# Optimization experiments

Hardware: AMD Instinct MI355X
Metric: run time of the kernel (lower is better)

## Reference

```python
import jax, jax.numpy as jnp
import numpy as np

D = 1024      # decoder_embed_dim
H = 16        # retention heads
DK = D // H   # q/k head dim = 64
DV = 2 * D // H  # value head dim = 128 (value_embed_dim = 2*embed_dim)
L = 3         # decoder layers
FFN = 4096
S = 1024      # seq len = Lx*Ly
B = 4
V = 2         # vocab
EPS = 1e-6


def layer_norm(x, s, b):
    m = x.mean(-1, keepdims=True)
    v = ((x - m) ** 2).mean(-1, keepdims=True)
    return (x - m) / jnp.sqrt(v + 1e-5) * s + b


def rotate_every_two(x):
    x1 = x[..., ::2]
    x2 = x[..., 1::2]
    return jnp.stack([-x2, x1], axis=-1).reshape(x.shape)


def rel_pos():
    # xpos-style rotary angles + per-head decay mask (torchscale RetNetRelPos)
    angle = 1.0 / (10000.0 ** jnp.linspace(0.0, 1.0, DK // 2))
    angle = jnp.stack([angle, angle], axis=-1).reshape(-1)  # [DK]
    idx = jnp.arange(S)
    sin = jnp.sin(idx[:, None] * angle[None, :])  # [S, DK]
    cos = jnp.cos(idx[:, None] * angle[None, :])
    gamma = 1.0 - 2.0 ** (-5.0 - jnp.arange(H, dtype=jnp.float32))  # [H]
    n = idx[:, None]
    m = idx[None, :]
    expo = jnp.where(n >= m, (n - m).astype(jnp.float32), 0.0)
    dmask = jnp.where(n >= m, gamma[:, None, None] ** expo[None], 0.0)  # [H,S,S]
    dmask = dmask / jnp.sqrt(dmask.sum(-1, keepdims=True))  # row-normalize
    dmask = jnp.nan_to_num(dmask)
    return sin, cos, dmask


def msr(x, Wq, Wk, Wv, Wg, Wo, sin, cos, dmask):
    # multi-scale retention, parallel form
    b, s, _ = x.shape
    q = (x @ Wq).reshape(b, s, H, DK)
    k = (x @ Wk).reshape(b, s, H, DK) * (DK ** -0.5)
    v = (x @ Wv).reshape(b, s, H, DV)
    c = cos[None, :, None, :]
    sn = sin[None, :, None, :]
    q = q * c + rotate_every_two(q) * sn
    k = k * c + rotate_every_two(k) * sn
    qk = jnp.einsum('bnhd,bmhd->bhnm', q, k) * dmask[None]  # [B,H,S,S]
    qk = qk / jnp.clip(jnp.abs(qk).sum(-1, keepdims=True), 1.0, None)
    o = jnp.einsum('bhnm,bmhd->bnhd', qk, v)  # [B,S,H,DV]
    # per-head RMS group norm, no affine
    o = o / jnp.sqrt((o ** 2).mean(-1, keepdims=True) + EPS)
    o = o.reshape(b, s, H * DV)
    o = jax.nn.silu(x @ Wg) * o  # swish gate
    return o @ Wo


def reference(tokens, emb, Wq, Wk, Wv, Wg, Wo, ln1_s, ln1_b, ln2_s, ln2_b,
              W1, b1, W2, b2, lnf_s, lnf_b, Wout):
    shifted = jnp.concatenate(
        [jnp.zeros((tokens.shape[0], 1), tokens.dtype), tokens[:, :-1]], axis=1)
    h = emb[shifted] * jnp.sqrt(jnp.float32(D))
    sin, cos, dmask = rel_pos()
    for l in range(L):
        h = h + msr(layer_norm(h, ln1_s[l], ln1_b[l]),
                    Wq[l], Wk[l], Wv[l], Wg[l], Wo[l], sin, cos, dmask)
        z = layer_norm(h, ln2_s[l], ln2_b[l])
        h = h + (jax.nn.gelu(z @ W1[l] + b1[l]) @ W2[l] + b2[l])
    h = layer_norm(h, lnf_s, lnf_b)
    logits = h @ Wout  # [B,S,V]
    return jax.nn.log_softmax(logits, axis=-1)


def setup_inputs() -> dict:
    key = jax.random.key(0)
    ks = jax.random.split(key, 12)
    sd = 0.02
    return {
        'tokens': jax.random.randint(ks[0], (B, S), 0, V),
        'emb': jax.random.normal(ks[1], (V, D), jnp.float32) * sd,
        'Wq': jax.random.normal(ks[2], (L, D, D), jnp.float32) * sd,
        'Wk': jax.random.normal(ks[3], (L, D, D), jnp.float32) * sd,
        'Wv': jax.random.normal(ks[4], (L, D, 2 * D), jnp.float32) * sd,
        'Wg': jax.random.normal(ks[5], (L, D, 2 * D), jnp.float32) * sd,
        'Wo': jax.random.normal(ks[6], (L, 2 * D, D), jnp.float32) * sd,
        'ln1_s': jnp.ones((L, D), jnp.float32),
        'ln1_b': jnp.zeros((L, D), jnp.float32),
        'ln2_s': jnp.ones((L, D), jnp.float32),
        'ln2_b': jnp.zeros((L, D), jnp.float32),
        'W1': jax.random.normal(ks[7], (L, D, FFN), jnp.float32) * sd,
        'b1': jnp.zeros((L, FFN), jnp.float32),
        'W2': jax.random.normal(ks[8], (L, FFN, D), jnp.float32) * sd,
        'b2': jnp.zeros((L, D), jnp.float32),
        'lnf_s': jnp.ones((D,), jnp.float32),
        'lnf_b': jnp.zeros((D,), jnp.float32),
        'Wout': jax.random.normal(ks[9], (D, V), jnp.float32) * sd,
    }
```

## Files before the change

### kernel.cpp

```cpp
#include <hip/hip_runtime.h>
#include <hip/hip_bf16.h>
#include <math.h>
#include <stdint.h>

#define D_   1024
#define H_   16
#define DK_  64
#define DV_  128
#define L_   3
#define FFN_ 4096
#define S_   1024
#define B_   4
#define NF_  6144

typedef __attribute__((ext_vector_type(8))) _Float16 f16x8;
typedef __attribute__((ext_vector_type(4))) _Float16 f16x4;
typedef __attribute__((ext_vector_type(4))) float f32x4;

__device__ __forceinline__ void gl2lds16(const void* g, void* l) {
    __builtin_amdgcn_global_load_lds(
        (const __attribute__((address_space(1))) void*)(uintptr_t)g,
        (__attribute__((address_space(3))) void*)(uintptr_t)l, 16, 0, 0);
}
#define MFMA16(a,b,c) __builtin_amdgcn_mfma_f32_16x16x32_f16(a,b,c,0,0,0)

__device__ __forceinline__ float fast_gelu(float v) {
    float y = 1.5957691216f * (v + 0.044715f * v * v * v);
    return v * (1.0f / (1.0f + __expf(-y)));
}

__device__ __forceinline__ void tile_swizzle(int pid, int N, int* m0, int* n0) {
    int nb = N >> 7;
    int sgn = nb >> 3;
    int sid = pid >> 6, wi = pid & 63;
    int smi = sid / sgn, sni = sid - smi * sgn;
    *m0 = ((smi << 3) + (wi >> 3)) << 7;
    *n0 = ((sni << 3) + (wi & 7)) << 7;
}

__global__ __launch_bounds__(256) void k_embed(const int* __restrict__ tokens,
                                               const float* __restrict__ emb,
                                               float* __restrict__ h) {
    int i = blockIdx.x * 256 + threadIdx.x;
    int d  = i & (D_ - 1);
    int bs = i >> 10;
    int s  = bs & (S_ - 1);
    int b  = bs >> 10;
    int tok = (s == 0) ? 0 : tokens[b * S_ + s - 1];
    h[i] = emb[tok * D_ + d] * 32.0f;
}

__global__ __launch_bounds__(256) void k_ln(float* __restrict__ x,
                                            const float* __restrict__ p0,
                                            const float* __restrict__ p1,
                                            int np,
                                            const float* __restrict__ s,
                                            const float* __restrict__ b,
                                            _Float16* __restrict__ y) {
    int row = blockIdx.x;
    int t = threadIdx.x;
    size_t base = (size_t)row * D_ + t * 4;
    float4 xv = *(float4*)&x[base];
    if (np) {
        float4 a = *(const float4*)&p0[base];
        float4 c = *(const float4*)&p1[base];
        xv.x += a.x + c.x; xv.y += a.y + c.y;
        xv.z += a.z + c.z; xv.w += a.w + c.w;
        *(float4*)&x[base] = xv;
    }
    float sum = xv.x + xv.y + xv.z + xv.w;
    float ssq = xv.x * xv.x + xv.y * xv.y + xv.z * xv.z + xv.w * xv.w;
    __shared__ float sm1[4], sm2[4];
    #pragma unroll
    for (int off = 32; off > 0; off >>= 1) {
        sum += __shfl_down(sum, off, 64);
        ssq += __shfl_down(ssq, off, 64);
    }
    int lane = t & 63, w = t >> 6;
    if (lane == 0) { sm1[w] = sum; sm2[w] = ssq; }
    __syncthreads();
    sum = sm1[0] + sm1[1] + sm1[2] + sm1[3];
    ssq = sm2[0] + sm2[1] + sm2[2] + sm2[3];
    float mean = sum * (1.0f / D_);
    float var  = ssq * (1.0f / D_) - mean * mean;
    float inv  = 1.0f / sqrtf(var + 1e-5f);
    float4 sv = *(const float4*)&s[t * 4];
    float4 bv = *(const float4*)&b[t * 4];
    f16x4 o;
    o.x = (_Float16)((xv.x - mean) * inv * sv.x + bv.x);
    o.y = (_Float16)((xv.y - mean) * inv * sv.y + bv.y);
    o.z = (_Float16)((xv.z - mean) * inv * sv.z + bv.z);
    o.w = (_Float16)((xv.w - mean) * inv * sv.w + bv.w);
    *(f16x4*)&y[base] = o;
}

__global__ __launch_bounds__(256) void k_wcast(const float* __restrict__ in,
                                               _Float16* __restrict__ out,
                                               int K, int N) {
    __shared__ float Ts[32][33];
    int n0 = blockIdx.x * 32, k0 = blockIdx.y * 32;
    int t = threadIdx.x;
    #pragma unroll
    for (int c = 0; c < 4; c++) {
        int e = c * 256 + t; int kr = e >> 5, nc = e & 31;
        Ts[kr][nc] = in[(size_t)(k0 + kr) * N + n0 + nc];
    }
    __syncthreads();
    #pragma unroll
    for (int c = 0; c < 4; c++) {
        int e = c * 256 + t; int nr = e >> 5, kc = e & 31;
        out[(size_t)(n0 + nr) * K + k0 + kc] = (_Float16)Ts[kc][nr];
    }
}

__global__ __launch_bounds__(256) void k_gemm_mfma(
    const _Float16* __restrict__ A, const _Float16* __restrict__ Bt,
    const float* __restrict__ bias, float* __restrict__ Cf,
    _Float16* __restrict__ Ch, int M, int N, int K, int flags)
{
    __shared__ __attribute__((aligned(16))) _Float16 As[128 * 32];
    __shared__ __attribute__((aligned(16))) _Float16 Bs[128 * 32];
    int t = threadIdx.x;
    int m0, n0;
    tile_swizzle(blockIdx.x, N, &m0, &n0);
    int w = t >> 6, lane = t & 63;
    int quad = lane >> 4, l16 = lane & 15;
    int wm = (w >> 1) * 64, wn = (w & 1) * 64;
    const f16x8* aptr[4]; const f16x8* bptr[4];
    #pragma unroll
    for (int i = 0; i < 4; i++) {
        int ra = wm + i * 16 + l16;
        aptr[i] = (const f16x8*)&As[ra * 32 + ((quad ^ ((ra >> 1) & 3)) * 8)];
        int rb = wn + i * 16 + l16;
        bptr[i] = (const f16x8*)&Bs[rb * 32 + ((quad ^ ((rb >> 1) & 3)) * 8)];
    }
    f32x4 acc[4][4] = {};
    for (int k0 = 0; k0 < K; k0 += 32) {
        __syncthreads();
        #pragma unroll
        for (int c = 0; c < 2; c++) {
            int chunk = c * 256 + t;
            int row = chunk >> 2, cg = chunk & 3;
            int ko = (cg ^ ((row >> 1) & 3)) * 8;
            gl2lds16(A  + (size_t)(m0 + row) * K + k0 + ko, As + chunk * 8);
            gl2lds16(Bt + (size_t)(n0 + row) * K + k0 + ko, Bs + chunk * 8);
        }
        __syncthreads();
        f16x8 af[4], bfr[4];
        #pragma unroll
        for (int i = 0; i < 4; i++) af[i] = *aptr[i];
        #pragma unroll
        for (int j = 0; j < 4; j++) bfr[j] = *bptr[j];
        #pragma unroll
        for (int i = 0; i < 4; i++)
            #pragma unroll
            for (int j = 0; j < 4; j++)
                acc[i][j] = MFMA16(af[i], bfr[j], acc[i][j]);
    }
    #pragma unroll
    for (int i = 0; i < 4; i++) {
        #pragma unroll
        for (int r = 0; r < 4; r++) {
            int row = m0 + wm + i * 16 + quad * 4 + r;
            #pragma unroll
            for (int j = 0; j < 4; j++) {
                int col = n0 + wn + j * 16 + l16;
                float v = acc[i][j][r];
                if (flags & 2) v += bias[col];
                if (flags & 4) v = fast_gelu(v);
                if (flags & 8) Ch[(size_t)row * N + col] = (_Float16)v;
                else Cf[(size_t)row * N + col] = v;
            }
        }
    }
}

__global__ __launch_bounds__(256) void k_gemm_splitk(
    const _Float16* __restrict__ A, const _Float16* __restrict__ Bt,
    const float* __restrict__ bias, float* __restrict__ P,
    int M, int N, int K, int Kc)
{
    __shared__ __attribute__((aligned(16))) _Float16 As[128 * 32];
    __shared__ __attribute__((aligned(16))) _Float16 Bs[128 * 32];
    int t = threadIdx.x;
    int m0, n0;
    tile_swizzle(blockIdx.x, N, &m0, &n0);
    int kc = blockIdx.z;
    const _Float16* Ac  = A  + (size_t)kc * Kc;
    const _Float16* Btc = Bt + (size_t)kc * Kc;
    float* Pz = P + (size_t)kc * M * N;
    int w = t >> 6, lane = t & 63;
    int quad = lane >> 4, l16 = lane & 15;
    int wm = (w >> 1) * 64, wn = (w & 1) * 64;
    const f16x8* aptr[4]; const f16x8* bptr[4];
    #pragma unroll
    for (int i = 0; i < 4; i++) {
        int ra = wm + i * 16 + l16;
        aptr[i] = (const f16x8*)&As[ra * 32 + ((quad ^ ((ra >> 1) & 3)) * 8)];
        int rb = wn + i * 16 + l16;
        bptr[i] = (const f16x8*)&Bs[rb * 32 + ((quad ^ ((rb >> 1) & 3)) * 8)];
    }
    f32x4 acc[4][4] = {};
    for (int k0 = 0; k0 < Kc; k0 += 32) {
        __syncthreads();
        #pragma unroll
        for (int c = 0; c < 2; c++) {
            int chunk = c * 256 + t;
            int row = chunk >> 2, cg = chunk & 3;
            int ko = (cg ^ ((row >> 1) & 3)) * 8;
            gl2lds16(Ac  + (size_t)(m0 + row) * K + k0 + ko, As + chunk * 8);
            gl2lds16(Btc + (size_t)(n0 + row) * K + k0 + ko, Bs + chunk * 8);
        }
        __syncthreads();
        f16x8 af[4], bfr[4];
        #pragma unroll
        for (int i = 0; i < 4; i++) af[i] = *aptr[i];
        #pragma unroll
        for (int j = 0; j < 4; j++) bfr[j] = *bptr[j];
        #pragma unroll
        for (int i = 0; i < 4; i++)
            #pragma unroll
            for (int j = 0; j < 4; j++)
                acc[i][j] = MFMA16(af[i], bfr[j], acc[i][j]);
    }
    bool addb = (kc == 0) && (bias != nullptr);
    #pragma unroll
    for (int i = 0; i < 4; i++) {
        #pragma unroll
        for (int r = 0; r < 4; r++) {
            int row = m0 + wm + i * 16 + quad * 4 + r;
            #pragma unroll
            for (int j = 0; j < 4; j++) {
                int col = n0 + wn + j * 16 + l16;
                float v = acc[i][j][r];
                if (addb) v += bias[col];
                Pz[(size_t)row * N + col] = v;
            }
        }
    }
}

__global__ __launch_bounds__(256) void k_rope(_Float16* __restrict__ x, float scale) {
    int i = blockIdx.x * 256 + threadIdx.x;
    int pair = i & 31;
    int hh = (i >> 5) & 15;
    int bs = i >> 9;
    int sIdx = bs & (S_ - 1);
    float ang = expf(-(float)pair * (1.0f / 31.0f) * 9.210340372f);
    float ph = (float)sIdx * ang;
    float sn, cs;
    sincosf(ph, &sn, &cs);
    size_t base = (size_t)bs * NF_ + hh * DK_ + 2 * pair;
    float x1 = (float)x[base], x2 = (float)x[base + 1];
    x[base]     = (_Float16)((x1 * cs - x2 * sn) * scale);
    x[base + 1] = (_Float16)((x2 * cs + x1 * sn) * scale);
}

__global__ __launch_bounds__(256) void k_vtrans(const _Float16* __restrict__ vb,
                                                _Float16* __restrict__ Vt) {
    int st = blockIdx.x, dt = blockIdx.y, bh = blockIdx.z;
    int hh = bh & 15, b = bh >> 4;
    __shared__ __attribute__((aligned(16))) _Float16 Ts[64][72];
    int t = threadIdx.x;
    const _Float16* src = vb + (size_t)(b * S_ + st * 64) * NF_ + 2048 + hh * DV_ + dt * 64;
    #pragma unroll
    for (int c = 0; c < 2; c++) {
        int chunk = c * 256 + t;
        int r = chunk >> 3, co = (chunk & 7) * 8;
        *(f16x8*)&Ts[r][co] = *(const f16x8*)(src + (size_t)r * NF_ + co);
    }
    __syncthreads();
    _Float16* dst = Vt + ((size_t)bh * DV_ + dt * 64) * S_ + st * 64;
    #pragma unroll
    for (int c = 0; c < 2; c++) {
        int chunk = c * 256 + t;
        int dr = chunk >> 3, so = (chunk & 7) * 8;
        f16x8 val;
        #pragma unroll
        for (int j = 0; j < 8; j++) val[j] = Ts[so + j][dr];
        *(f16x8*)(dst + (size_t)dr * S_ + so) = val;
    }
}

__global__ __launch_bounds__(256) void k_attn(const _Float16* __restrict__ qkvg,
                                              const _Float16* __restrict__ Vt,
                                              float* __restrict__ of) {
    int nt = blockIdx.x, bh = blockIdx.y;
    int hh = bh & 15, b = bh >> 4;
    int t = threadIdx.x, w = t >> 6, lane = t & 63;
    int quad = lane >> 4, l16 = lane & 15;
    int n0 = nt * 64;

    __shared__ __attribute__((aligned(16))) _Float16 Qs[64 * 64];
    __shared__ __attribute__((aligned(16))) _Float16 Ks[64 * 64];
    __shared__ __attribute__((aligned(16))) _Float16 Vs[128 * 64];
    __shared__ __attribute__((aligned(16))) _Float16 Ss[64 * 64];

    const _Float16* qg = qkvg + (size_t)(b * S_ + n0) * NF_ + hh * DK_;
    const _Float16* kg = qkvg + (size_t)(b * S_) * NF_ + 1024 + hh * DK_;
    const _Float16* vg = Vt + (size_t)bh * DV_ * S_;

    #pragma unroll
    for (int c = 0; c < 2; c++) {
        int chunk = c * 256 + t;
        int r = chunk >> 3, cg = chunk & 7;
        int ko = (cg ^ (r & 7)) * 8;
        gl2lds16(qg + (size_t)r * NF_ + ko, Qs + chunk * 8);
    }
    double gd   = 1.0 - exp2((double)(-5 - hh));
    double l2gd = log2(gd);
    float  l2g  = (float)l2gd;
    float rn[4];
    #pragma unroll
    for (int r = 0; r < 4; r++) {
        int n = n0 + w * 16 + quad * 4 + r;
        double rowsum = (1.0 - exp2(l2gd * (double)(n + 1))) / (1.0 - gd);
        rn[r] = (float)(1.0 / sqrt(rowsum));
    }
    int ra = w * 16 + l16;
    const f16x8* qp0 = (const f16x8*)&Qs[ra * 64 + (( quad      ^ (ra & 7)) * 8)];
    const f16x8* qp1 = (const f16x8*)&Qs[ra * 64 + (((quad + 4) ^ (ra & 7)) * 8)];
    const f16x8* sp0 = (const f16x8*)&Ss[ra * 64 + (( quad      ^ (ra & 7)) * 8)];
    const f16x8* sp1 = (const f16x8*)&Ss[ra * 64 + (((quad + 4) ^ (ra & 7)) * 8)];
    const f16x8* kp0[4]; const f16x8* kp1[4];
    const f16x8* vp0[8]; const f16x8* vp1[8];
    #pragma unroll
    for (int j = 0; j < 4; j++) {
        int rb = j * 16 + l16;
        kp0[j] = (const f16x8*)&Ks[rb * 64 + (( quad      ^ (rb & 7)) * 8)];
        kp1[j] = (const f16x8*)&Ks[rb * 64 + (((quad + 4) ^ (rb & 7)) * 8)];
    }
    #pragma unroll
    for (int j = 0; j < 8; j++) {
        int rv = j * 16 + l16;
        vp0[j] = (const f16x8*)&Vs[rv * 64 + (( quad      ^ (rv & 7)) * 8)];
        vp1[j] = (const f16x8*)&Vs[rv * 64 + (((quad + 4) ^ (rv & 7)) * 8)];
    }
    f32x4 oacc[8] = {};
    float absAcc[4] = {};

    for (int mt = 0; mt <= nt; mt++) {
        int m0 = mt * 64;
        __syncthreads();
        #pragma unroll
        for (int c = 0; c < 2; c++) {
            int chunk = c * 256 + t;
            int r = chunk >> 3, cg = chunk & 7;
            int ko = (cg ^ (r & 7)) * 8;
            gl2lds16(kg + (size_t)(m0 + r) * NF_ + ko, Ks + chunk * 8);
        }
        #pragma unroll
        for (int c = 0; c < 4; c++) {
            int chunk = c * 256 + t;
            int r = chunk >> 3, cg = chunk & 7;
            int ko = (cg ^ (r & 7)) * 8;
            gl2lds16(vg + (size_t)r * S_ + m0 + ko, Vs + chunk * 8);
        }
        __syncthreads();
        f16x8 a0 = *qp0, a1 = *qp1;
        f32x4 sacc[4] = {};
        #pragma unroll
        for (int j = 0; j < 4; j++) {
            sacc[j] = MFMA16(a0, *kp0[j], sacc[j]);
            sacc[j] = MFMA16(a1, *kp1[j], sacc[j]);
        }
        #pragma unroll
        for (int j = 0; j < 4; j++) {
            int m = m0 + j * 16 + l16;
            #pragma unroll
            for (int r = 0; r < 4; r++) {
                int n = n0 + w * 16 + quad * 4 + r;
                float dm = (n >= m) ? exp2f((float)(n - m) * l2g) * rn[r] : 0.0f;
                float sv = sacc[j][r] * dm;
                absAcc[r] += fabsf(sv);
                int rowS = w * 16 + quad * 4 + r;
                int colS = j * 16 + l16;
                Ss[rowS * 64 + ((((colS >> 3) ^ (rowS & 7)) << 3) | (colS & 7))] = (_Float16)sv;
            }
        }
        __syncthreads();
        f16x8 s0 = *sp0, s1 = *sp1;
        #pragma unroll
        for (int j = 0; j < 8; j++) {
            oacc[j] = MFMA16(s0, *vp0[j], oacc[j]);
            oacc[j] = MFMA16(s1, *vp1[j], oacc[j]);
        }
    }
    #pragma unroll
    for (int r = 0; r < 4; r++) {
        float s_ = absAcc[r];
        #pragma unroll
        for (int off = 1; off < 16; off <<= 1) s_ += __shfl_xor(s_, off, 64);
        absAcc[r] = s_;
    }
    #pragma unroll
    for (int r = 0; r < 4; r++) {
        int n = n0 + w * 16 + quad * 4 + r;
        float sc = 1.0f / fmaxf(absAcc[r], 1.0f);
        float* og = of + (size_t)(b * S_ + n) * (H_ * DV_) + hh * DV_;
        #pragma unroll
        for (int j = 0; j < 8; j++)
            og[j * 16 + l16] = oacc[j][r] * sc;
    }
}

__global__ __launch_bounds__(256) void k_rmsgate(const float* __restrict__ o,
                                                 const _Float16* __restrict__ qkvg,
                                                 _Float16* __restrict__ out) {
    int row = blockIdx.x * 2 + (threadIdx.x >> 7);
    int tc = threadIdx.x & 127;
    int bs = row >> 4, hh = row & 15;
    size_t obase = (size_t)row * 128 + tc;
    float val = o[obase];
    float gv  = (float)qkvg[(size_t)bs * NF_ + 4096 + hh * DV_ + tc];
    float ss = val * val;
    #pragma unroll
    for (int off = 32; off > 0; off >>= 1) ss += __shfl_down(ss, off, 64);
    __shared__ float sm[4];
    int wv = threadIdx.x >> 6;
    if ((threadIdx.x & 63) == 0) sm[wv] = ss;
    __syncthreads();
    int rw = (threadIdx.x >> 7) * 2;
    ss = sm[rw] + sm[rw + 1];
    float rms = 1.0f / sqrtf(ss * (1.0f / 128.0f) + 1e-6f);
    float sig = 1.0f / (1.0f + __expf(-gv));
    out[obase] = (_Float16)(gv * sig * val * rms);
}

__global__ __launch_bounds__(256) void k_final(const float* __restrict__ x,
                                               const float* __restrict__ p0,
                                               const float* __restrict__ p1,
                                               const float* __restrict__ s,
                                               const float* __restrict__ b,
                                               const float* __restrict__ Wout,
                                               float* __restrict__ out) {
    int row = blockIdx.x;
    int t = threadIdx.x;
    size_t base = (size_t)row * D_ + t * 4;
    float4 xv = *(const float4*)&x[base];
    {
        float4 a = *(const float4*)&p0[base];
        float4 c = *(const float4*)&p1[base];
        xv.x += a.x + c.x; xv.y += a.y + c.y;
        xv.z += a.z + c.z; xv.w += a.w + c.w;
    }
    float sum = xv.x + xv.y + xv.z + xv.w;
    float ssq = xv.x * xv.x + xv.y * xv.y + xv.z * xv.z + xv.w * xv.w;
    __shared__ float sm1[4], sm2[4];
    #pragma unroll
    for (int off = 32; off > 0; off >>= 1) {
        sum += __shfl_down(sum, off, 64);
        ssq += __shfl_down(ssq, off, 64);
    }
    int lane = t & 63, w = t >> 6;
    if (lane == 0) { sm1[w] = sum; sm2[w] = ssq; }
    __syncthreads();
    sum = sm1[0] + sm1[1] + sm1[2] + sm1[3];
    ssq = sm2[0] + sm2[1] + sm2[2] + sm2[3];
    float mean = sum * (1.0f / D_);
    float var  = ssq * (1.0f / D_) - mean * mean;
    float inv  = 1.0f / sqrtf(var + 1e-5f);
    float4 sv = *(const float4*)&s[t * 4];
    float4 bv = *(const float4*)&b[t * 4];
    float ln[4];
    ln[0] = (xv.x - mean) * inv * sv.x + bv.x;
    ln[1] = (xv.y - mean) * inv * sv.y + bv.y;
    ln[2] = (xv.z - mean) * inv * sv.z + bv.z;
    ln[3] = (xv.w - mean) * inv * sv.w + bv.w;
    float l0 = 0.0f, l1 = 0.0f;
    #pragma unroll
    for (int i = 0; i < 4; i++) {
        int d = t * 4 + i;
        l0 += ln[i] * Wout[d * 2 + 0];
        l1 += ln[i] * Wout[d * 2 + 1];
    }
    #pragma unroll
    for (int off = 32; off > 0; off >>= 1) {
        l0 += __shfl_down(l0, off, 64);
        l1 += __shfl_down(l1, off, 64);
    }
    __syncthreads();
    if (lane == 0) { sm1[w] = l0; sm2[w] = l1; }
    __syncthreads();
    if (t == 0) {
        l0 = sm1[0] + sm1[1] + sm1[2] + sm1[3];
        l1 = sm2[0] + sm2[1] + sm2[2] + sm2[3];
        float mx  = fmaxf(l0, l1);
        float lse = mx + logf(expf(l0 - mx) + expf(l1 - mx));
        out[(size_t)row * 2 + 0] = l0 - lse;
        out[(size_t)row * 2 + 1] = l1 - lse;
    }
}

extern "C" void kernel_launch(void* const* d_in, const int* in_sizes, int n_in,
                              void* d_out, int out_size, void* d_ws, size_t ws_size,
                              hipStream_t stream) {
    const int*   tokens = (const int*)d_in[0];
    const float* emb    = (const float*)d_in[1];
    const float* Wq     = (const float*)d_in[2];
    const float* Wk     = (const float*)d_in[3];
    const float* Wv     = (const float*)d_in[4];
    const float* Wg     = (const float*)d_in[5];
    const float* Wo     = (const float*)d_in[6];
    const float* ln1_s  = (const float*)d_in[7];
    const float* ln1_b  = (const float*)d_in[8];
    const float* ln2_s  = (const float*)d_in[9];
    const float* ln2_b  = (const float*)d_in[10];
    const float* W1     = (const float*)d_in[11];
    const float* b1     = (const float*)d_in[12];
    const float* W2     = (const float*)d_in[13];
    const float* b2     = (const float*)d_in[14];
    const float* lnf_s  = (const float*)d_in[15];
    const float* lnf_b  = (const float*)d_in[16];
    const float* Wout   = (const float*)d_in[17];

    float* ws = (float*)d_ws;
    const size_t M1 = 1u << 20;
    float*     h    = ws;
    _Float16*  x1h  = (_Float16*)(ws + 4 * M1);
    _Float16*  whb  = (_Float16*)(ws + 6 * M1);
    _Float16*  wQKVG= whb;
    _Float16*  woT  = whb + 6 * M1;
    _Float16*  w1T  = whb + 8 * M1;
    _Float16*  w2T  = whb + 12 * M1;
    _Float16*  qkvg = (_Float16*)(ws + 14 * M1);
    _Float16*  Vth  = (_Float16*)(ws + 27 * M1);
    float*     of   = ws + 31 * M1;
    _Float16*  oh   = (_Float16*)(ws + 27 * M1);
    _Float16*  f1h  = (_Float16*)(ws + 14 * M1);
    float*     pb0  = ws + 31 * M1;
    float*     pb1  = ws + 35 * M1;

    k_embed<<<16384, 256, 0, stream>>>(tokens, emb, h);

    for (int l = 0; l < L_; l++) {
        const float* pWq = Wq + (size_t)l * M1;
        const float* pWk = Wk + (size_t)l * M1;
        const float* pWv = Wv + (size_t)l * 2 * M1;
        const float* pWg = Wg + (size_t)l * 2 * M1;
        const float* pWo = Wo + (size_t)l * 2 * M1;
        const float* pW1 = W1 + (size_t)l * 4 * M1;
        const float* pW2 = W2 + (size_t)l * 4 * M1;

        k_wcast<<<dim3(32, 32),  256, 0, stream>>>(pWq, wQKVG,          1024, 1024);
        k_wcast<<<dim3(32, 32),  256, 0, stream>>>(pWk, wQKVG + 1 * M1, 1024, 1024);
        k_wcast<<<dim3(64, 32),  256, 0, stream>>>(pWv, wQKVG + 2 * M1, 1024, 2048);
        k_wcast<<<dim3(64, 32),  256, 0, stream>>>(pWg, wQKVG + 4 * M1, 1024, 2048);
        k_wcast<<<dim3(32, 64),  256, 0, stream>>>(pWo, woT, 2048, 1024);
        k_wcast<<<dim3(128, 32), 256, 0, stream>>>(pW1, w1T, 1024, 4096);
        k_wcast<<<dim3(32, 128), 256, 0, stream>>>(pW2, w2T, 4096, 1024);

        k_ln<<<4096, 256, 0, stream>>>(h, pb0, pb1, (l == 0) ? 0 : 1,
                                       ln1_s + l * D_, ln1_b + l * D_, x1h);
        k_gemm_mfma<<<dim3(1536), 256, 0, stream>>>(x1h, wQKVG, nullptr, nullptr, qkvg,
                                                    4096, NF_, 1024, 8);
        k_rope<<<8192, 256, 0, stream>>>(qkvg, 1.0f);
        k_rope<<<8192, 256, 0, stream>>>(qkvg + 1024, 0.125f);
        k_vtrans<<<dim3(16, 2, 64), 256, 0, stream>>>(qkvg, Vth);
        k_attn<<<dim3(16, 64), 256, 0, stream>>>(qkvg, Vth, of);
        k_rmsgate<<<32768, 256, 0, stream>>>(of, qkvg, oh);
        k_gemm_splitk<<<dim3(256, 1, 2), 256, 0, stream>>>(oh, woT, nullptr, pb0,
                                                           4096, 1024, 2048, 1024);
        k_ln<<<4096, 256, 0, stream>>>(h, pb0, pb1, 1,
                                       ln2_s + l * D_, ln2_b + l * D_, x1h);
        k_gemm_mfma<<<dim3(1024), 256, 0, stream>>>(x1h, w1T, b1 + l * FFN_, nullptr, f1h,
                                                    4096, 4096, 1024, 2 | 4 | 8);
        k_gemm_splitk<<<dim3(256, 1, 2), 256, 0, stream>>>(f1h, w2T, b2 + l * D_, pb0,
                                                           4096, 1024, 4096, 2048);
    }
    k_final<<<4096, 256, 0, stream>>>(h, pb0, pb1, lnf_s, lnf_b, Wout, (float*)d_out);
}
```

Before: 1.459 ms.

## Fuse rope into QKV GEMM, rmsgate into attention, residual into output GEMMs

```diff
diff --git a/kernel.cpp b/kernel.cpp
--- a/kernel.cpp
+++ b/kernel.cpp
@@ -50,24 +50,14 @@
     h[i] = emb[tok * D_ + d] * 32.0f;
 }
 
-__global__ __launch_bounds__(256) void k_ln(float* __restrict__ x,
-                                            const float* __restrict__ p0,
-                                            const float* __restrict__ p1,
-                                            int np,
+__global__ __launch_bounds__(256) void k_ln(const float* __restrict__ x,
                                             const float* __restrict__ s,
                                             const float* __restrict__ b,
                                             _Float16* __restrict__ y) {
     int row = blockIdx.x;
     int t = threadIdx.x;
     size_t base = (size_t)row * D_ + t * 4;
-    float4 xv = *(float4*)&x[base];
-    if (np) {
-        float4 a = *(const float4*)&p0[base];
-        float4 c = *(const float4*)&p1[base];
-        xv.x += a.x + c.x; xv.y += a.y + c.y;
-        xv.z += a.z + c.z; xv.w += a.w + c.w;
-        *(float4*)&x[base] = xv;
-    }
+    float4 xv = *(const float4*)&x[base];
     float sum = xv.x + xv.y + xv.z + xv.w;
     float ssq = xv.x * xv.x + xv.y * xv.y + xv.z * xv.z + xv.w * xv.w;
     __shared__ float sm1[4], sm2[4];
@@ -94,6 +84,34 @@
     *(f16x4*)&y[base] = o;
 }
 
+__global__ __launch_bounds__(256) void k_wcast4(const float* __restrict__ wq,
+                                                const float* __restrict__ wk,
+                                                const float* __restrict__ wv,
+                                                const float* __restrict__ wg,
+                                                _Float16* __restrict__ dst) {
+    int bid = blockIdx.x;
+    const float* src; _Float16* out; int N; int local;
+    if (bid < 1024)      { src = wq; out = dst;                 N = 1024; local = bid; }
+    else if (bid < 2048) { src = wk; out = dst + 1024 * 1024;   N = 1024; local = bid - 1024; }
+    else if (bid < 4096) { src = wv; out = dst + 2*1024*1024;   N = 2048; local = bid - 2048; }
+    else                 { src = wg; out = dst + 4*1024*1024;   N = 2048; local = bid - 4096; }
+    int ntiles = N >> 5;
+    int n0 = (local % ntiles) * 32, k0 = (local / ntiles) * 32;
+    __shared__ float Ts[32][33];
+    int t = threadIdx.x;
+    #pragma unroll
+    for (int c = 0; c < 4; c++) {
+        int e = c * 256 + t; int kr = e >> 5, nc = e & 31;
+        Ts[kr][nc] = src[(size_t)(k0 + kr) * N + n0 + nc];
+    }
+    __syncthreads();
+    #pragma unroll
+    for (int c = 0; c < 4; c++) {
+        int e = c * 256 + t; int nr = e >> 5, kc = e & 31;
+        out[(size_t)(n0 + nr) * 1024 + k0 + kc] = (_Float16)Ts[kc][nr];
+    }
+}
+
 __global__ __launch_bounds__(256) void k_wcast(const float* __restrict__ in,
                                                _Float16* __restrict__ out,
                                                int K, int N) {
@@ -115,8 +133,8 @@
 
 __global__ __launch_bounds__(256) void k_gemm_mfma(
     const _Float16* __restrict__ A, const _Float16* __restrict__ Bt,
-    const float* __restrict__ bias, float* __restrict__ Cf,
-    _Float16* __restrict__ Ch, int M, int N, int K, int flags)
+    const float* __restrict__ bias, _Float16* __restrict__ Ch,
+    int M, int N, int K, int flags)
 {
     __shared__ __attribute__((aligned(16))) _Float16 As[128 * 32];
     __shared__ __attribute__((aligned(16))) _Float16 Bs[128 * 32];
@@ -168,64 +186,78 @@
                 float v = acc[i][j][r];
                 if (flags & 2) v += bias[col];
                 if (flags & 4) v = fast_gelu(v);
-                if (flags & 8) Ch[(size_t)row * N + col] = (_Float16)v;
-                else Cf[(size_t)row * N + col] = v;
+                if (flags & 16) {
+                    if (col < 2048) {
+                        int p = (col & 63) >> 1;
+                        int srow = row & (S_ - 1);
+                        float ang = __expf(-(float)p * (1.0f / 31.0f) * 9.210340372f);
+                        float ph = (float)srow * ang;
+                        float sn, cs;
+                        __sincosf(ph, &sn, &cs);
+                        float partner = __shfl_xor(v, 1, 64);
+                        v = (l16 & 1) ? (v * cs + partner * sn)
+                                      : (v * cs - partner * sn);
+                        if (col >= 1024) v *= 0.125f;
+                    }
+                }
+                Ch[(size_t)row * N + col] = (_Float16)v;
             }
         }
     }
 }
 
-__global__ __launch_bounds__(256) void k_gemm_splitk(
+__global__ __launch_bounds__(256) void k_gemm_rmw(
     const _Float16* __restrict__ A, const _Float16* __restrict__ Bt,
-    const float* __restrict__ bias, float* __restrict__ P,
-    int M, int N, int K, int Kc)
+    const float* __restrict__ bias, float* __restrict__ Cf,
+    int M, int N, int K)
 {
-    __shared__ __attribute__((aligned(16))) _Float16 As[128 * 32];
+    __shared__ __attribute__((aligned(16))) _Float16 As[64 * 32];
     __shared__ __attribute__((aligned(16))) _Float16 Bs[128 * 32];
     int t = threadIdx.x;
-    int m0, n0;
-    tile_swizzle(blockIdx.x, N, &m0, &n0);
-    int kc = blockIdx.z;
-    const _Float16* Ac  = A  + (size_t)kc * Kc;
-    const _Float16* Btc = Bt + (size_t)kc * Kc;
-    float* Pz = P + (size_t)kc * M * N;
+    int n0 = blockIdx.x * 128, m0 = blockIdx.y * 64;
     int w = t >> 6, lane = t & 63;
     int quad = lane >> 4, l16 = lane & 15;
-    int wm = (w >> 1) * 64, wn = (w & 1) * 64;
-    const f16x8* aptr[4]; const f16x8* bptr[4];
-    #pragma unroll
-    for (int i = 0; i < 4; i++) {
+    int wm = (w >> 1) * 32, wn = (w & 1) * 64;
+    const f16x8* aptr[2]; const f16x8* bptr[4];
+    #pragma unroll
+    for (int i = 0; i < 2; i++) {
         int ra = wm + i * 16 + l16;
         aptr[i] = (const f16x8*)&As[ra * 32 + ((quad ^ ((ra >> 1) & 3)) * 8)];
-        int rb = wn + i * 16 + l16;
-        bptr[i] = (const f16x8*)&Bs[rb * 32 + ((quad ^ ((rb >> 1) & 3)) * 8)];
-    }
-    f32x4 acc[4][4] = {};
-    for (int k0 = 0; k0 < Kc; k0 += 32) {
-        __syncthreads();
+    }
+    #pragma unroll
+    for (int j = 0; j < 4; j++) {
+        int rb = wn + j * 16 + l16;
+        bptr[j] = (const f16x8*)&Bs[rb * 32 + ((quad ^ ((rb >> 1) & 3)) * 8)];
+    }
+    f32x4 acc[2][4] = {};
+    for (int k0 = 0; k0 < K; k0 += 32) {
+        __syncthreads();
+        {
+            int row = t >> 2, cg = t & 3;
+            int ko = (cg ^ ((row >> 1) & 3)) * 8;
+            gl2lds16(A + (size_t)(m0 + row) * K + k0 + ko, As + t * 8);
+        }
         #pragma unroll
         for (int c = 0; c < 2; c++) {
             int chunk = c * 256 + t;
             int row = chunk >> 2, cg = chunk & 3;
             int ko = (cg ^ ((row >> 1) & 3)) * 8;
-            gl2lds16(Ac  + (size_t)(m0 + row) * K + k0 + ko, As + chunk * 8);
-            gl2lds16(Btc + (size_t)(n0 + row) * K + k0 + ko, Bs + chunk * 8);
-        }
-        __syncthreads();
-        f16x8 af[4], bfr[4];
-        #pragma unroll
-        for (int i = 0; i < 4; i++) af[i] = *aptr[i];
+            gl2lds16(Bt + (size_t)(n0 + row) * K + k0 + ko, Bs + chunk * 8);
+        }
+        __syncthreads();
+        f16x8 af[2], bfr[4];
+        #pragma unroll
+        for (int i = 0; i < 2; i++) af[i] = *aptr[i];
         #pragma unroll
         for (int j = 0; j < 4; j++) bfr[j] = *bptr[j];
         #pragma unroll
-        for (int i = 0; i < 4; i++)
+        for (int i = 0; i < 2; i++)
             #pragma unroll
             for (int j = 0; j < 4; j++)
                 acc[i][j] = MFMA16(af[i], bfr[j], acc[i][j]);
     }
-    bool addb = (kc == 0) && (bias != nullptr);
-    #pragma unroll
-    for (int i = 0; i < 4; i++) {
+    #pragma unroll
+    for (int i = 0; i < 2; i++) {
         #pragma unroll
         for (int r = 0; r < 4; r++) {
             int row = m0 + wm + i * 16 + quad * 4 + r;
@@ -233,27 +265,12 @@
             for (int j = 0; j < 4; j++) {
                 int col = n0 + wn + j * 16 + l16;
                 float v = acc[i][j][r];
-                if (addb) v += bias[col];
-                Pz[(size_t)row * N + col] = v;
+                if (bias) v += bias[col];
+                size_t idx = (size_t)row * N + col;
+                Cf[idx] += v;
             }
         }
     }
-}
-
-__global__ __launch_bounds__(256) void k_rope(_Float16* __restrict__ x, float scale) {
-    int i = blockIdx.x * 256 + threadIdx.x;
-    int pair = i & 31;
-    int hh = (i >> 5) & 15;
-    int bs = i >> 9;
-    int sIdx = bs & (S_ - 1);
-    float ang = expf(-(float)pair * (1.0f / 31.0f) * 9.210340372f);
-    float ph = (float)sIdx * ang;
-    float sn, cs;
-    sincosf(ph, &sn, &cs);
-    size_t base = (size_t)bs * NF_ + hh * DK_ + 2 * pair;
-    float x1 = (float)x[base], x2 = (float)x[base + 1];
-    x[base]     = (_Float16)((x1 * cs - x2 * sn) * scale);
-    x[base + 1] = (_Float16)((x2 * cs + x1 * sn) * scale);
 }
 
 __global__ __launch_bounds__(256) void k_vtrans(const _Float16* __restrict__ vb,
@@ -284,7 +301,7 @@
 
 __global__ __launch_bounds__(256) void k_attn(const _Float16* __restrict__ qkvg,
                                               const _Float16* __restrict__ Vt,
-                                              float* __restrict__ of) {
+                                              _Float16* __restrict__ oh) {
     int nt = blockIdx.x, bh = blockIdx.y;
     int hh = bh & 15, b = bh >> 4;
     int t = threadIdx.x, w = t >> 6, lane = t & 63;
@@ -397,39 +414,28 @@
     for (int r = 0; r < 4; r++) {
         int n = n0 + w * 16 + quad * 4 + r;
         float sc = 1.0f / fmaxf(absAcc[r], 1.0f);
-        float* og = of + (size_t)(b * S_ + n) * (H_ * DV_) + hh * DV_;
-        #pragma unroll
-        for (int j = 0; j < 8; j++)
-            og[j * 16 + l16] = oacc[j][r] * sc;
-    }
-}
-
-__global__ __launch_bounds__(256) void k_rmsgate(const float* __restrict__ o,
-                                                 const _Float16* __restrict__ qkvg,
-                                                 _Float16* __restrict__ out) {
-    int row = blockIdx.x * 2 + (threadIdx.x >> 7);
-    int tc = threadIdx.x & 127;
-    int bs = row >> 4, hh = row & 15;
-    size_t obase = (size_t)row * 128 + tc;
-    float val = o[obase];
-    float gv  = (float)qkvg[(size_t)bs * NF_ + 4096 + hh * DV_ + tc];
-    float ss = val * val;
-    #pragma unroll
-    for (int off = 32; off > 0; off >>= 1) ss += __shfl_down(ss, off, 64);
-    __shared__ float sm[4];
-    int wv = threadIdx.x >> 6;
-    if ((threadIdx.x & 63) == 0) sm[wv] = ss;
-    __syncthreads();
-    int rw = (threadIdx.x >> 7) * 2;
-    ss = sm[rw] + sm[rw + 1];
-    float rms = 1.0f / sqrtf(ss * (1.0f / 128.0f) + 1e-6f);
-    float sig = 1.0f / (1.0f + __expf(-gv));
-    out[obase] = (_Float16)(gv * sig * val * rms);
+        float vals[8];
+        float ssq = 0.0f;
+        #pragma unroll
+        for (int j = 0; j < 8; j++) {
+            vals[j] = oacc[j][r] * sc;
+            ssq += vals[j] * vals[j];
+        }
+        #pragma unroll
+        for (int off = 1; off < 16; off <<= 1) ssq += __shfl_xor(ssq, off, 64);
+        float rms = 1.0f / sqrtf(ssq * (1.0f / 128.0f) + 1e-6f);
+        const _Float16* gg = qkvg + (size_t)(b * S_ + n) * NF_ + 4096 + hh * DV_;
+        _Float16* og = oh + (size_t)(b * S_ + n) * (H_ * DV_) + hh * DV_;
+        #pragma unroll
+        for (int j = 0; j < 8; j++) {
+            float gv = (float)gg[j * 16 + l16];
+            float sig = 1.0f / (1.0f + __expf(-gv));
+            og[j * 16 + l16] = (_Float16)(gv * sig * vals[j] * rms);
+        }
+    }
 }
 
 __global__ __launch_bounds__(256) void k_final(const float* __restrict__ x,
-                                               const float* __restrict__ p0,
-                                               const float* __restrict__ p1,
                                                const float* __restrict__ s,
                                                const float* __restrict__ b,
                                                const float* __restrict__ Wout,
@@ -438,12 +444,6 @@
     int t = threadIdx.x;
     size_t base = (size_t)row * D_ + t * 4;
     float4 xv = *(const float4*)&x[base];
-    {
-        float4 a = *(const float4*)&p0[base];
-        float4 c = *(const float4*)&p1[base];
-        xv.x += a.x + c.x; xv.y += a.y + c.y;
-        xv.z += a.z + c.z; xv.w += a.w + c.w;
-    }
     float sum = xv.x + xv.y + xv.z + xv.w;
     float ssq = xv.x * xv.x + xv.y * xv.y + xv.z * xv.z + xv.w * xv.w;
     __shared__ float sm1[4], sm2[4];
@@ -525,11 +525,8 @@
     _Float16*  w2T  = whb + 12 * M1;
     _Float16*  qkvg = (_Float16*)(ws + 14 * M1);
     _Float16*  Vth  = (_Float16*)(ws + 27 * M1);
-    float*     of   = ws + 31 * M1;
-    _Float16*  oh   = (_Float16*)(ws + 27 * M1);
+    _Float16*  oh   = (_Float16*)(ws + 31 * M1);
     _Float16*  f1h  = (_Float16*)(ws + 14 * M1);
-    float*     pb0  = ws + 31 * M1;
-    float*     pb1  = ws + 35 * M1;
 
     k_embed<<<16384, 256, 0, stream>>>(tokens, emb, h);
 
@@ -542,31 +539,23 @@
         const float* pW1 = W1 + (size_t)l * 4 * M1;
         const float* pW2 = W2 + (size_t)l * 4 * M1;
 
-        k_wcast<<<dim3(32, 32),  256, 0, stream>>>(pWq, wQKVG,          1024, 1024);
-        k_wcast<<<dim3(32, 32),  256, 0, stream>>>(pWk, wQKVG + 1 * M1, 1024, 1024);
-        k_wcast<<<dim3(64, 32),  256, 0, stream>>>(pWv, wQKVG + 2 * M1, 1024, 2048);
-        k_wcast<<<dim3(64, 32),  256, 0, stream>>>(pWg, wQKVG + 4 * M1, 1024, 2048);
+        k_wcast4<<<6144, 256, 0, stream>>>(pWq, pWk, pWv, pWg, wQKVG);
         k_wcast<<<dim3(32, 64),  256, 0, stream>>>(pWo, woT, 2048, 1024);
         k_wcast<<<dim3(128, 32), 256, 0, stream>>>(pW1, w1T, 1024, 4096);
         k_wcast<<<dim3(32, 128), 256, 0, stream>>>(pW2, w2T, 4096, 1024);
 
-        k_ln<<<4096, 256, 0, stream>>>(h, pb0, pb1, (l == 0) ? 0 : 1,
-                                       ln1_s + l * D_, ln1_b + l * D_, x1h);
-        k_gemm_mfma<<<dim3(1536), 256, 0, stream>>>(x1h, wQKVG, nullptr, nullptr, qkvg,
-                                                    4096, NF_, 1024, 8);
-        k_rope<<<8192, 256, 0, stream>>>(qkvg, 1.0f);
-        k_rope<<<8192, 256, 0, stream>>>(qkvg + 1024, 0.125f);
+        k_ln<<<4096, 256, 0, stream>>>(h, ln1_s + l * D_, ln1_b + l * D_, x1h);
+        k_gemm_mfma<<<dim3(1536), 256, 0, stream>>>(x1h, wQKVG, nullptr, qkvg,
+                                                    4096, NF_, 1024, 16);
         k_vtrans<<<dim3(16, 2, 64), 256, 0, stream>>>(qkvg, Vth);
-        k_attn<<<dim3(16, 64), 256, 0, stream>>>(qkvg, Vth, of);
-        k_rmsgate<<<32768, 256, 0, stream>>>(of, qkvg, oh);
-        k_gemm_splitk<<<dim3(256, 1, 2), 256, 0, stream>>>(oh, woT, nullptr, pb0,
-                                                           4096, 1024, 2048, 1024);
-        k_ln<<<4096, 256, 0, stream>>>(h, pb0, pb1, 1,
-                                       ln2_s + l * D_, ln2_b + l * D_, x1h);
-        k_gemm_mfma<<<dim3(1024), 256, 0, stream>>>(x1h, w1T, b1 + l * FFN_, nullptr, f1h,
-                                                    4096, 4096, 1024, 2 | 4 | 8);
-        k_gemm_splitk<<<dim3(256, 1, 2), 256, 0, stream>>>(f1h, w2T, b2 + l * D_, pb0,
-                                                           4096, 1024, 4096, 2048);
-    }
-    k_final<<<4096, 256, 0, stream>>>(h, pb0, pb1, lnf_s, lnf_b, Wout, (float*)d_out);
-}
+        k_attn<<<dim3(16, 64), 256, 0, stream>>>(qkvg, Vth, oh);
+        k_gemm_rmw<<<dim3(8, 64), 256, 0, stream>>>(oh, woT, nullptr, h,
+                                                    4096, 1024, 2048);
+        k_ln<<<4096, 256, 0, stream>>>(h, ln2_s + l * D_, ln2_b + l * D_, x1h);
+        k_gemm_mfma<<<dim3(1024), 256, 0, stream>>>(x1h, w1T, b1 + l * FFN_, f1h,
+                                                    4096, 4096, 1024, 2 | 4);
+        k_gemm_rmw<<<dim3(8, 64), 256, 0, stream>>>(f1h, w2T, b2 + l * D_, h,
+                                                    4096, 1024, 4096);
+    }
+    k_final<<<4096, 256, 0, stream>>>(h, lnf_s, lnf_b, Wout, (float*)d_out);
+}
```

After: 1.443 ms. About the same (-1.1%).
